# Kernel tuning notes

Hardware: AMD Instinct MI355X
Metric: run time of the kernel (lower is better)

The kernel has to match this reference:

```python
import jax, jax.numpy as jnp
import numpy as np

N_U = 200000
N_I = 100000
DIM = 128
N_E = 1500000
N_LAYERS = 2


def setup_inputs() -> dict:
    key = jax.random.key(0)
    k1, k2, k3, k4 = jax.random.split(key, 4)
    # xavier-uniform-ish init (bounded values); exact init scheme irrelevant for kernel correctness
    bound = float(np.sqrt(6.0 / (N_U + DIM)))
    u_emb = jax.random.uniform(k1, (N_U, DIM), jnp.float32, -bound, bound)
    bound_i = float(np.sqrt(6.0 / (N_I + DIM)))
    i_emb = jax.random.uniform(k2, (N_I, DIM), jnp.float32, -bound_i, bound_i)
    u_idx = jax.random.randint(k3, (N_E,), 0, N_U, dtype=jnp.int64 if jax.config.jax_enable_x64 else jnp.int32)
    i_idx = jax.random.randint(k4, (N_E,), 0, N_I, dtype=jnp.int64 if jax.config.jax_enable_x64 else jnp.int32)
    return {"u_emb": u_emb, "i_emb": i_emb, "u_idx": u_idx, "i_idx": i_idx}


def _prop(x, r, c, n):
    # symmetric-normalized gather-scale-scatter (SpMM), as in _LightGCN._prop
    deg = jnp.bincount(jnp.concatenate([r, c]), length=n).astype(x.dtype)
    norm = (jnp.clip(deg[r], 1e-10) ** -0.5) * (jnp.clip(deg[c], 1e-10) ** -0.5)  # [2E]
    msg = x[c] * norm[:, None]  # [2E, dim]
    return jax.ops.segment_sum(msg, r, num_segments=n)


def reference(u_emb, i_emb, u_idx, i_idx):
    n_u = u_emb.shape[0]
    n = n_u + i_emb.shape[0]
    it = i_idx + n_u
    r = jnp.concatenate([u_idx, it])  # row (destination) indices
    c = jnp.concatenate([it, u_idx])  # col (source) indices
    x = jnp.concatenate([u_emb, i_emb], axis=0)  # [n, dim]
    outs = [x]
    for _ in range(N_LAYERS):
        x = _prop(x, r, c, n)
        outs.append(x)
    fin = jnp.mean(jnp.stack(outs), axis=0)
    return (fin[:n_u], fin[n_u:])
```

## Files before the change

kernel.cpp:

```cpp
#include <hip/hip_runtime.h>

#define DIM 128
#define NBLK 256
#define BKT_BITS 9
#define BKT_ROWS 512
#define MAXBUK 1024

using f16 = _Float16;
using f16x4 = __attribute__((ext_vector_type(4))) f16;
using f32x4 = __attribute__((ext_vector_type(4))) float;


__device__ __forceinline__ int permb(int b) { return ((b & 7) << 5) | (b >> 3); }

__global__ __launch_bounds__(256) void k_hist(const int* __restrict__ u_idx,
                                              const int* __restrict__ i_idx,
                                              int E, int n_u, int NBUK,
                                              int* __restrict__ hist) {
    __shared__ int h[MAXBUK];
    int b = blockIdx.x, tid = threadIdx.x;
    for (int j = tid; j < NBUK; j += 256) h[j] = 0;
    __syncthreads();
    int chunk = (E + NBLK - 1) / NBLK;
    int i0 = b * chunk, i1 = E < i0 + chunk ? E : i0 + chunk;
    for (int i = i0 + tid; i < i1; i += 256) {
        int u = __builtin_nontemporal_load(&u_idx[i]);
        int t = __builtin_nontemporal_load(&i_idx[i]) + n_u;
        atomicAdd(&h[u >> BKT_BITS], 1);
        atomicAdd(&h[t >> BKT_BITS], 1);
    }
    __syncthreads();
    int pb = permb(b);
    for (int j = tid; j < NBUK; j += 256) hist[j * NBLK + pb] = h[j];
}

__global__ __launch_bounds__(256) void k_scanB(int* __restrict__ hist,
                                               int* __restrict__ bb) {
    __shared__ int sh[256];
    int k = blockIdx.x, t = threadIdx.x;
    int v = hist[k * NBLK + t];
    sh[t] = v;
    __syncthreads();
    for (int off = 1; off < 256; off <<= 1) {
        int tmp = (t >= off) ? sh[t - off] : 0;
        __syncthreads();
        sh[t] += tmp;
        __syncthreads();
    }
    hist[k * NBLK + t] = sh[t] - v;
    if (t == 255) bb[k] = sh[255];
}

__global__ __launch_bounds__(1024) void k_scanT(int* __restrict__ bb, int NBUK) {
    __shared__ int sh[1024];
    int t = threadIdx.x;
    int v = (t < NBUK) ? bb[t] : 0;
    sh[t] = v;
    __syncthreads();
    for (int off = 1; off < 1024; off <<= 1) {
        int tmp = (t >= off) ? sh[t - off] : 0;
        __syncthreads();
        sh[t] += tmp;
        __syncthreads();
    }
    if (t < NBUK) bb[t] = sh[t] - v;
    if (t == NBUK - 1) bb[NBUK] = sh[t];
}

__global__ __launch_bounds__(256) void k_scatter(const int* __restrict__ u_idx,
                                                 const int* __restrict__ i_idx,
                                                 int E, int n_u, int NBUK,
                                                 const int* __restrict__ hist,
                                                 const int* __restrict__ bb,
                                                 unsigned* __restrict__ pre) {
    __shared__ int boff[MAXBUK];
    __shared__ int cnt[MAXBUK];
    int b = blockIdx.x, tid = threadIdx.x;
    int pb = permb(b);
    for (int j = tid; j < NBUK; j += 256) {
        boff[j] = bb[j] + hist[j * NBLK + pb];
        cnt[j] = 0;
    }
    __syncthreads();
    int chunk = (E + NBLK - 1) / NBLK;
    int i0 = b * chunk, i1 = E < i0 + chunk ? E : i0 + chunk;
    for (int i = i0 + tid; i < i1; i += 256) {
        int u = __builtin_nontemporal_load(&u_idx[i]);
        int t = __builtin_nontemporal_load(&i_idx[i]) + n_u;
        int ku = u >> BKT_BITS, kt = t >> BKT_BITS;
        int p1 = atomicAdd(&cnt[ku], 1);
        pre[boff[ku] + p1] = ((unsigned)t << BKT_BITS) | (unsigned)(u & (BKT_ROWS - 1));
        int p2 = atomicAdd(&cnt[kt], 1);
        pre[boff[kt] + p2] = ((unsigned)u << BKT_BITS) | (unsigned)(t & (BKT_ROWS - 1));
    }
}

__global__ __launch_bounds__(256) void k_place(const int* __restrict__ bb, int n,
                                               const unsigned* __restrict__ pre,
                                               int* __restrict__ row_ptr,
                                               int* __restrict__ adj) {
    __shared__ int cnt[BKT_ROWS];
    __shared__ int cur[BKT_ROWS];
    __shared__ int ps[256];
    int b = blockIdx.x, t = threadIdx.x;
    int r0 = b << BKT_BITS;
    int base = bb[b], end = bb[b + 1];
    cnt[t] = 0;
    cnt[t + 256] = 0;
    __syncthreads();
    for (int i = base + t; i < end; i += 256)
        atomicAdd(&cnt[pre[i] & (BKT_ROWS - 1)], 1);
    __syncthreads();
    int a0 = cnt[2 * t], a1 = cnt[2 * t + 1];
    int pv = a0 + a1;
    ps[t] = pv;
    __syncthreads();
    for (int off = 1; off < 256; off <<= 1) {
        int tmp = (t >= off) ? ps[t - off] : 0;
        __syncthreads();
        ps[t] += tmp;
        __syncthreads();
    }
    int ex = ps[t] - pv;
    int e0 = base + ex;
    int e1 = e0 + a0;
    cur[2 * t] = e0;
    cur[2 * t + 1] = e1;
    int rows = n - r0; if (rows > BKT_ROWS) rows = BKT_ROWS;
    if (2 * t < rows)     row_ptr[r0 + 2 * t] = e0;
    if (2 * t + 1 < rows) row_ptr[r0 + 2 * t + 1] = e1;
    if (t == 0 && r0 + BKT_ROWS >= n) row_ptr[n] = end;
    __syncthreads();
    for (int i = base + t; i < end; i += 256) {
        unsigned p = pre[i];
        int rl = (int)(p & (BKT_ROWS - 1));
        int c = (int)(p >> BKT_BITS);
        int pos = atomicAdd(&cur[rl], 1);
        adj[pos] = c;
    }
}

__global__ void k_scale_h(const float* __restrict__ u_emb, const float* __restrict__ i_emb,
                          const int* __restrict__ row_ptr, float* __restrict__ rnorm,
                          int n_u, int n, f16* __restrict__ xh) {
    int g = blockIdx.x * blockDim.x + threadIdx.x;
    int stride = gridDim.x * blockDim.x;
    int total = n * 32;
    for (; g < total; g += stride) {
        int v = g >> 5;
        int lane = g & 31;
        int d = row_ptr[v + 1] - row_ptr[v];
        float r = (d > 0) ? rsqrtf(2.0f * (float)d) : 0.0f;
        if (lane == 0) rnorm[v] = r;
        const float* src = (v < n_u) ? (u_emb + (size_t)v * DIM)
                                     : (i_emb + (size_t)(v - n_u) * DIM);
        f32x4 x = __builtin_nontemporal_load(
            reinterpret_cast<const f32x4*>(src + lane * 4));
        f16x4 o;
        o[0] = (f16)(x[0] * r);
        o[1] = (f16)(x[1] * r);
        o[2] = (f16)(x[2] * r);
        o[3] = (f16)(x[3] * r);
        *reinterpret_cast<f16x4*>(xh + (size_t)v * DIM + lane * 4) = o;
    }
}


template <int MODE>
__global__ __launch_bounds__(256) void k_spmm(const int* __restrict__ row_ptr,
                                              const int* __restrict__ adj,
                                              const float* __restrict__ rnorm,
                                              const f16* __restrict__ xh,
                                              const float* __restrict__ u_emb,
                                              const float* __restrict__ i_emb,
                                              int n_u, int n,
                                              float* __restrict__ y,
                                              f16* __restrict__ yh) {
    int g = blockIdx.x * blockDim.x + threadIdx.x;
    int row = g >> 5;
    int lane = g & 31;
    if (row >= n) return;
    int s = row_ptr[row];
    int e = row_ptr[row + 1];
    float rnr = rnorm[row];
    f32x4 acc = {0.f, 0.f, 0.f, 0.f};
    const f16* xb = xh + lane * 4;
    int e1 = e - 1;
    for (int k = s; k < e; k += 4) {
        int k1 = k + 1, k2 = k + 2, k3 = k + 3;
        int c0 = adj[k];
        int c1 = adj[(k1 <= e1) ? k1 : e1];
        int c2 = adj[(k2 <= e1) ? k2 : e1];
        int c3 = adj[(k3 <= e1) ? k3 : e1];
        float w1 = (k1 < e) ? 1.f : 0.f;
        float w2 = (k2 < e) ? 1.f : 0.f;
        float w3 = (k3 < e) ? 1.f : 0.f;
        f16x4 v0 = *reinterpret_cast<const f16x4*>(xb + (size_t)c0 * DIM);
        f16x4 v1 = *reinterpret_cast<const f16x4*>(xb + (size_t)c1 * DIM);
        f16x4 v2 = *reinterpret_cast<const f16x4*>(xb + (size_t)c2 * DIM);
        f16x4 v3 = *reinterpret_cast<const f16x4*>(xb + (size_t)c3 * DIM);
        acc[0] += (float)v0[0];
        acc[1] += (float)v0[1];
        acc[2] += (float)v0[2];
        acc[3] += (float)v0[3];
        acc[0] = fmaf((float)v1[0], w1, acc[0]);
        acc[1] = fmaf((float)v1[1], w1, acc[1]);
        acc[2] = fmaf((float)v1[2], w1, acc[2]);
        acc[3] = fmaf((float)v1[3], w1, acc[3]);
        acc[0] = fmaf((float)v2[0], w2, acc[0]);
        acc[1] = fmaf((float)v2[1], w2, acc[1]);
        acc[2] = fmaf((float)v2[2], w2, acc[2]);
        acc[3] = fmaf((float)v2[3], w2, acc[3]);
        acc[0] = fmaf((float)v3[0], w3, acc[0]);
        acc[1] = fmaf((float)v3[1], w3, acc[1]);
        acc[2] = fmaf((float)v3[2], w3, acc[2]);
        acc[3] = fmaf((float)v3[3], w3, acc[3]);
    }
    if (MODE == 0) {
        float sc = rnr * rnr;
        f16x4 h;
        h[0] = (f16)(acc[0] * sc);
        h[1] = (f16)(acc[1] * sc);
        h[2] = (f16)(acc[2] * sc);
        h[3] = (f16)(acc[3] * sc);
        *reinterpret_cast<f16x4*>(yh + (size_t)row * DIM + lane * 4) = h;
    } else {
        const float* x0b = (row < n_u) ? (u_emb + (size_t)row * DIM)
                                       : (i_emb + (size_t)(row - n_u) * DIM);
        f32x4 x0 = __builtin_nontemporal_load(
            reinterpret_cast<const f32x4*>(x0b + lane * 4));
        f16x4 a1 = *reinterpret_cast<const f16x4*>(xh + (size_t)row * DIM + lane * 4);
        float inv = (rnr > 0.f) ? (1.0f / rnr) : 0.f;
        const float third = 1.0f / 3.0f;
        f32x4 o;
        o[0] = (x0[0] + (float)a1[0] * inv + acc[0] * rnr) * third;
        o[1] = (x0[1] + (float)a1[1] * inv + acc[1] * rnr) * third;
        o[2] = (x0[2] + (float)a1[2] * inv + acc[2] * rnr) * third;
        o[3] = (x0[3] + (float)a1[3] * inv + acc[3] * rnr) * third;
        __builtin_nontemporal_store(
            o, reinterpret_cast<f32x4*>(y + (size_t)row * DIM + lane * 4));
    }
}


static inline int grid_for(long long work, int block, int cap = 4096) {
    long long b = (work + block - 1) / block;
    if (b > cap) b = cap;
    if (b < 1) b = 1;
    return (int)b;
}

extern "C" void kernel_launch(void* const* d_in, const int* in_sizes, int n_in,
                              void* d_out, int out_size, void* d_ws, size_t ws_size,
                              hipStream_t stream) {
    const float* u_emb = (const float*)d_in[0];
    const float* i_emb = (const float*)d_in[1];
    const int* u_idx = (const int*)d_in[2];
    const int* i_idx = (const int*)d_in[3];

    const int n_u = in_sizes[0] / DIM;
    const int n_i = in_sizes[1] / DIM;
    const int n = n_u + n_i;
    const int E = in_sizes[2];
    const int twoE = 2 * E;
    const int NBUK = (n + BKT_ROWS - 1) >> BKT_BITS;

    char* w = (char*)d_ws;
    auto alloc = [&](size_t bytes) -> void* {
        void* p = (void*)w;
        w += (bytes + 255) & ~(size_t)255;
        return p;
    };
    f16*   xh0     = (f16*)alloc((size_t)n * DIM * sizeof(f16));
    f16*   xh1     = (f16*)alloc((size_t)n * DIM * sizeof(f16));
    float* rnorm   = (float*)alloc((size_t)n * sizeof(float));
    int*   row_ptr = (int*)alloc((size_t)(n + 1) * sizeof(int));
    int*   adj     = (int*)alloc((size_t)twoE * sizeof(int));
    int*   hist    = (int*)alloc((size_t)NBUK * NBLK * sizeof(int));
    int*   bb      = (int*)alloc((size_t)(NBUK + 1) * sizeof(int));
    unsigned* pre  = (unsigned*)xh1;
    (void)ws_size;

    k_hist<<<NBLK, 256, 0, stream>>>(u_idx, i_idx, E, n_u, NBUK, hist);
    k_scanB<<<NBUK, 256, 0, stream>>>(hist, bb);
    k_scanT<<<1, 1024, 0, stream>>>(bb, NBUK);
    k_scatter<<<NBLK, 256, 0, stream>>>(u_idx, i_idx, E, n_u, NBUK, hist, bb, pre);
    k_place<<<NBUK, 256, 0, stream>>>(bb, n, pre, row_ptr, adj);
    k_scale_h<<<grid_for((long long)n * 32, 256, 8192), 256, 0, stream>>>(u_emb, i_emb,
                                                                          row_ptr, rnorm,
                                                                          n_u, n, xh0);

    int sblocks = (int)(((long long)n * 32 + 255) / 256);
    k_spmm<0><<<sblocks, 256, 0, stream>>>(row_ptr, adj, rnorm, xh0, nullptr, nullptr,
                                           n_u, n, nullptr, xh1);
    k_spmm<1><<<sblocks, 256, 0, stream>>>(row_ptr, adj, rnorm, xh1, u_emb, i_emb,
                                           n_u, n, (float*)d_out, nullptr);
}
```

Before: 379.3 us.

## Fuse normalization and fp16 scaling into k_place; reuse scaled fp16 x0 in final layer

Folds the per-row degree normalization and fp16 pre-scaling of the input embeddings into the CSR placement kernel. Degrees now come from shared-memory counts rather than row_ptr, which removes one kernel launch and the row_ptr reread. The final SpMM pass now rebuilds x0 from the fp16 scaled copy (xh0) instead of reloading the fp32 embeddings, which halves that read traffic. The fp32 embeddings are still read for zero-degree rows. The trade-off is extra fp16 rounding error on the x0 term.

```diff
diff --git a/kernel.cpp b/kernel.cpp
--- a/kernel.cpp
+++ b/kernel.cpp
@@ -95,10 +95,14 @@
     }
 }
 
-__global__ __launch_bounds__(256) void k_place(const int* __restrict__ bb, int n,
+__global__ __launch_bounds__(256) void k_place(const int* __restrict__ bb, int n, int n_u,
                                                const unsigned* __restrict__ pre,
+                                               const float* __restrict__ u_emb,
+                                               const float* __restrict__ i_emb,
                                                int* __restrict__ row_ptr,
-                                               int* __restrict__ adj) {
+                                               float* __restrict__ rnorm,
+                                               int* __restrict__ adj,
+                                               f16* __restrict__ xh0) {
     __shared__ int cnt[BKT_ROWS];
     __shared__ int cur[BKT_ROWS];
     __shared__ int ps[256];
@@ -127,8 +131,14 @@
     cur[2 * t] = e0;
     cur[2 * t + 1] = e1;
     int rows = n - r0; if (rows > BKT_ROWS) rows = BKT_ROWS;
-    if (2 * t < rows)     row_ptr[r0 + 2 * t] = e0;
-    if (2 * t + 1 < rows) row_ptr[r0 + 2 * t + 1] = e1;
+    if (2 * t < rows) {
+        row_ptr[r0 + 2 * t] = e0;
+        rnorm[r0 + 2 * t] = (a0 > 0) ? rsqrtf(2.0f * (float)a0) : 0.0f;
+    }
+    if (2 * t + 1 < rows) {
+        row_ptr[r0 + 2 * t + 1] = e1;
+        rnorm[r0 + 2 * t + 1] = (a1 > 0) ? rsqrtf(2.0f * (float)a1) : 0.0f;
+    }
     if (t == 0 && r0 + BKT_ROWS >= n) row_ptr[n] = end;
     __syncthreads();
     for (int i = base + t; i < end; i += 256) {
@@ -138,20 +148,12 @@
         int pos = atomicAdd(&cur[rl], 1);
         adj[pos] = c;
     }
-}
-
-__global__ void k_scale_h(const float* __restrict__ u_emb, const float* __restrict__ i_emb,
-                          const int* __restrict__ row_ptr, float* __restrict__ rnorm,
-                          int n_u, int n, f16* __restrict__ xh) {
-    int g = blockIdx.x * blockDim.x + threadIdx.x;
-    int stride = gridDim.x * blockDim.x;
-    int total = n * 32;
-    for (; g < total; g += stride) {
-        int v = g >> 5;
+    for (int g = t; g < rows * 32; g += 256) {
+        int vr = g >> 5;
         int lane = g & 31;
-        int d = row_ptr[v + 1] - row_ptr[v];
+        int v = r0 + vr;
+        int d = cnt[vr];
         float r = (d > 0) ? rsqrtf(2.0f * (float)d) : 0.0f;
-        if (lane == 0) rnorm[v] = r;
         const float* src = (v < n_u) ? (u_emb + (size_t)v * DIM)
                                      : (i_emb + (size_t)(v - n_u) * DIM);
         f32x4 x = __builtin_nontemporal_load(
@@ -161,7 +163,7 @@
         o[1] = (f16)(x[1] * r);
         o[2] = (f16)(x[2] * r);
         o[3] = (f16)(x[3] * r);
-        *reinterpret_cast<f16x4*>(xh + (size_t)v * DIM + lane * 4) = o;
+        *reinterpret_cast<f16x4*>(xh0 + (size_t)v * DIM + lane * 4) = o;
     }
 }
 
@@ -171,6 +173,7 @@
                                               const int* __restrict__ adj,
                                               const float* __restrict__ rnorm,
                                               const f16* __restrict__ xh,
+                                              const f16* __restrict__ xh0e,
                                               const float* __restrict__ u_emb,
                                               const float* __restrict__ i_emb,
                                               int n_u, int n,
@@ -225,30 +228,30 @@
         h[3] = (f16)(acc[3] * sc);
         *reinterpret_cast<f16x4*>(yh + (size_t)row * DIM + lane * 4) = h;
     } else {
-        const float* x0b = (row < n_u) ? (u_emb + (size_t)row * DIM)
-                                       : (i_emb + (size_t)(row - n_u) * DIM);
-        f32x4 x0 = __builtin_nontemporal_load(
-            reinterpret_cast<const f32x4*>(x0b + lane * 4));
-        f16x4 a1 = *reinterpret_cast<const f16x4*>(xh + (size_t)row * DIM + lane * 4);
-        float inv = (rnr > 0.f) ? (1.0f / rnr) : 0.f;
         const float third = 1.0f / 3.0f;
         f32x4 o;
-        o[0] = (x0[0] + (float)a1[0] * inv + acc[0] * rnr) * third;
-        o[1] = (x0[1] + (float)a1[1] * inv + acc[1] * rnr) * third;
-        o[2] = (x0[2] + (float)a1[2] * inv + acc[2] * rnr) * third;
-        o[3] = (x0[3] + (float)a1[3] * inv + acc[3] * rnr) * third;
+        if (rnr > 0.f) {
+            f16x4 a0v = *reinterpret_cast<const f16x4*>(xh0e + (size_t)row * DIM + lane * 4);
+            f16x4 a1v = *reinterpret_cast<const f16x4*>(xh + (size_t)row * DIM + lane * 4);
+            float inv = 1.0f / rnr;
+            o[0] = (((float)a0v[0] + (float)a1v[0]) * inv + acc[0] * rnr) * third;
+            o[1] = (((float)a0v[1] + (float)a1v[1]) * inv + acc[1] * rnr) * third;
+            o[2] = (((float)a0v[2] + (float)a1v[2]) * inv + acc[2] * rnr) * third;
+            o[3] = (((float)a0v[3] + (float)a1v[3]) * inv + acc[3] * rnr) * third;
+        } else {
+            const float* x0b = (row < n_u) ? (u_emb + (size_t)row * DIM)
+                                           : (i_emb + (size_t)(row - n_u) * DIM);
+            f32x4 x0 = *reinterpret_cast<const f32x4*>(x0b + lane * 4);
+            o[0] = x0[0] * third;
+            o[1] = x0[1] * third;
+            o[2] = x0[2] * third;
+            o[3] = x0[3] * third;
+        }
         __builtin_nontemporal_store(
             o, reinterpret_cast<f32x4*>(y + (size_t)row * DIM + lane * 4));
     }
 }
 
-
-static inline int grid_for(long long work, int block, int cap = 4096) {
-    long long b = (work + block - 1) / block;
-    if (b > cap) b = cap;
-    if (b < 1) b = 1;
-    return (int)b;
-}
 
 extern "C" void kernel_launch(void* const* d_in, const int* in_sizes, int n_in,
                               void* d_out, int out_size, void* d_ws, size_t ws_size,
@@ -285,14 +288,12 @@
     k_scanB<<<NBUK, 256, 0, stream>>>(hist, bb);
     k_scanT<<<1, 1024, 0, stream>>>(bb, NBUK);
     k_scatter<<<NBLK, 256, 0, stream>>>(u_idx, i_idx, E, n_u, NBUK, hist, bb, pre);
-    k_place<<<NBUK, 256, 0, stream>>>(bb, n, pre, row_ptr, adj);
-    k_scale_h<<<grid_for((long long)n * 32, 256, 8192), 256, 0, stream>>>(u_emb, i_emb,
-                                                                          row_ptr, rnorm,
-                                                                          n_u, n, xh0);
+    k_place<<<NBUK, 256, 0, stream>>>(bb, n, n_u, pre, u_emb, i_emb,
+                                      row_ptr, rnorm, adj, xh0);
 
     int sblocks = (int)(((long long)n * 32 + 255) / 256);
-    k_spmm<0><<<sblocks, 256, 0, stream>>>(row_ptr, adj, rnorm, xh0, nullptr, nullptr,
-                                           n_u, n, nullptr, xh1);
-    k_spmm<1><<<sblocks, 256, 0, stream>>>(row_ptr, adj, rnorm, xh1, u_emb, i_emb,
-                                           n_u, n, (float*)d_out, nullptr);
-}
+    k_spmm<0><<<sblocks, 256, 0, stream>>>(row_ptr, adj, rnorm, xh0, nullptr,
+                                           nullptr, nullptr, n_u, n, nullptr, xh1);
+    k_spmm<1><<<sblocks, 256, 0, stream>>>(row_ptr, adj, rnorm, xh1, xh0,
+                                           u_emb, i_emb, n_u, n, (float*)d_out, nullptr);
+}
```

New measurement: 384.5 us. Within noise of the previous version (+1.4%).
